# Kernel optimization log

Hardware: AMD Instinct MI355X
Metric: run time of the kernel (lower is better)

## Reference

```python
import jax, jax.numpy as jnp
import numpy as np

R = 16            # DFL bins (reg_max)
C = 80            # num classes
STRIDES = (8, 16, 32)
CONF = 0.25
IOU_T = 0.45
MAX_DET = 300
K_PRE = 1024      # fixed pre-NMS candidate count (static-shape stand-in for torch's boolean mask)
CLS_OFFSET = 4096.0  # > max image coord; class-aware NMS offset (torchvision batched_nms trick)


def setup_inputs() -> dict:
    key = jax.random.key(0)
    k0, k1, k2 = jax.random.split(key, 3)
    B, CH = 16, 4 * R + C
    return {
        "p0": jax.random.normal(k0, (B, CH, 80, 80), jnp.float32),
        "p1": jax.random.normal(k1, (B, CH, 40, 40), jnp.float32),
        "p2": jax.random.normal(k2, (B, CH, 20, 20), jnp.float32),
        "h_img": 640,
        "w_img": 640,
    }


def _decode_level(p, stride):
    # p: (B, 4R+C, H, W)
    B, _, H, W = p.shape
    box_logits = p[:, : 4 * R].reshape(B, 4, R, H * W)
    bins = jnp.arange(R, dtype=p.dtype)
    # DFLIntegral: softmax over bins, expectation -> l,t,r,b distances (in stride units)
    ltrb = jnp.einsum('bkrm,r->bkm', jax.nn.softmax(box_logits, axis=2), bins) * stride  # (B,4,HW)
    yv, xv = jnp.meshgrid(jnp.arange(H, dtype=p.dtype), jnp.arange(W, dtype=p.dtype), indexing='ij')
    cx = (xv.reshape(-1) + 0.5) * stride  # (HW,)
    cy = (yv.reshape(-1) + 0.5) * stride
    x1 = cx[None] - ltrb[:, 0]
    y1 = cy[None] - ltrb[:, 1]
    x2 = cx[None] + ltrb[:, 2]
    y2 = cy[None] + ltrb[:, 3]
    boxes = jnp.stack((x1, y1, x2, y2), axis=2)  # (B, HW, 4)
    scores = jax.nn.sigmoid(p[:, 4 * R:].reshape(B, C, H * W))  # (B, C, HW)
    smax = scores.max(axis=1)      # (B, HW)
    labels = scores.argmax(axis=1)  # (B, HW) int
    return boxes, smax, labels


def _pairwise_iou(b):
    # b: (K, 4) xyxy
    area = (b[:, 2] - b[:, 0]) * (b[:, 3] - b[:, 1])
    lt = jnp.maximum(b[:, None, :2], b[None, :, :2])
    rb = jnp.minimum(b[:, None, 2:], b[None, :, 2:])
    wh = jnp.clip(rb - lt, 0.0)
    inter = wh[..., 0] * wh[..., 1]
    return inter / (area[:, None] + area[None, :] - inter + 1e-7)


def _nms_single(boxes, smax, labels):
    # boxes (A,4), smax (A,), labels (A,)
    s = jnp.where(smax > CONF, smax, -1.0)
    sv, idx = jax.lax.top_k(s, K_PRE)          # score-sorted pre-NMS candidates
    bsel = boxes[idx]                           # (K,4)
    lsel = labels[idx]
    vsel = sv > CONF                            # candidate passes conf filter
    boff = bsel + lsel[:, None].astype(bsel.dtype) * CLS_OFFSET  # class-aware offset
    iou = _pairwise_iou(boff)
    iou = iou * (1.0 - jnp.eye(K_PRE, dtype=iou.dtype))  # no self-suppression

    def step(supp, i):
        keep_i = jnp.logical_and(~supp[i], vsel[i])
        supp = jnp.where(keep_i, supp | (iou[i] > IOU_T), supp)
        return supp, keep_i

    _, keep = jax.lax.scan(step, jnp.zeros(K_PRE, bool), jnp.arange(K_PRE))
    rank = jnp.cumsum(keep) - 1
    slot = jnp.where(keep & (rank < MAX_DET), rank, MAX_DET)  # dump overflow into dummy slot
    boxes_out = jnp.zeros((MAX_DET + 1, 4), bsel.dtype).at[slot].set(bsel)[:MAX_DET]
    scores_out = jnp.zeros((MAX_DET + 1,), sv.dtype).at[slot].set(sv)[:MAX_DET]
    labels_out = jnp.full((MAX_DET + 1,), -1, jnp.int32).at[slot].set(lsel.astype(jnp.int32))[:MAX_DET]
    n = jnp.minimum(keep.sum(), MAX_DET)
    valid_out = jnp.arange(MAX_DET) < n
    return boxes_out, scores_out, labels_out, valid_out


def reference(p0, p1, p2, h_img, w_img):
    parts = [_decode_level(p, s) for p, s in zip((p0, p1, p2), STRIDES)]
    boxes = jnp.concatenate([x[0] for x in parts], axis=1)   # (B, A, 4)
    smax = jnp.concatenate([x[1] for x in parts], axis=1)    # (B, A)
    labels = jnp.concatenate([x[2] for x in parts], axis=1)  # (B, A)
    hi = jnp.array([w_img - 1, h_img - 1, w_img - 1, h_img - 1], boxes.dtype)
    boxes = jnp.clip(boxes, 0.0, hi)
    return jax.vmap(_nms_single)(boxes, smax, labels)
```

## Files before the change

### kernel.cpp

```cpp
#include <hip/hip_runtime.h>
#include <stdint.h>

#define NR 16
#define NC 80
#define NA 8400
#define NB 16
#define KPRE 1024
#define MAXDET 300
#define CONF_T 0.25f
#define IOU_THR 0.45f

__device__ __forceinline__ float read_dim(const void* p) {
  int iv = *(const int*)p;
  return (iv > 0 && iv < (1 << 20)) ? (float)iv : *(const float*)p;
}

__device__ __forceinline__ const float* level_ptr(const float* p0, const float* p1,
                                                  const float* p2, int a, int& HW,
                                                  int& W, float& stride, int& m) {
  if (a < 6400)      { HW = 6400; W = 80; stride = 8.f;  m = a;        return p0; }
  else if (a < 8000) { HW = 1600; W = 40; stride = 16.f; m = a - 6400; return p1; }
  else               { HW = 400;  W = 20; stride = 32.f; m = a - 8000; return p2; }
}

__device__ __forceinline__ uint64_t readlane64(uint64_t v, int lane) {
  uint32_t lo = (uint32_t)__builtin_amdgcn_readlane((int)(uint32_t)v, lane);
  uint32_t hi = (uint32_t)__builtin_amdgcn_readlane((int)(uint32_t)(v >> 32), lane);
  return ((uint64_t)hi << 32) | lo;
}

__global__ __launch_bounds__(256) void k_decode(
    const float* __restrict__ p0, const float* __restrict__ p1,
    const float* __restrict__ p2, const void* __restrict__ hp,
    const void* __restrict__ wp, float4* __restrict__ boxes,
    uint32_t* __restrict__ keys, int* __restrict__ labels) {
  int gid = blockIdx.x * 256 + threadIdx.x;
  if (gid >= NB * NA) return;
  int b = gid / NA, a = gid - b * NA;
  int HW, W, m; float stride;
  const float* p = level_ptr(p0, p1, p2, a, HW, W, stride, m);
  const float* base = p + (size_t)b * (4 * NR + NC) * HW + m;

  float d[4];
#pragma unroll
  for (int k = 0; k < 4; ++k) {
    float v[NR]; float mx = -3.4e38f;
#pragma unroll
    for (int r = 0; r < NR; ++r) { v[r] = base[(size_t)(k * NR + r) * HW]; mx = fmaxf(mx, v[r]); }
    float se = 0.f, sn = 0.f;
#pragma unroll
    for (int r = 0; r < NR; ++r) { float e = expf(v[r] - mx); se += e; sn += e * (float)r; }
    d[k] = sn / se * stride;
  }
  int x = m % W, y = m / W;
  float cx = ((float)x + 0.5f) * stride, cy = ((float)y + 0.5f) * stride;
  float hx = read_dim(wp) - 1.f, hy = read_dim(hp) - 1.f;
  boxes[gid] = make_float4(fminf(fmaxf(cx - d[0], 0.f), hx),
                           fminf(fmaxf(cy - d[1], 0.f), hy),
                           fminf(fmaxf(cx + d[2], 0.f), hx),
                           fminf(fmaxf(cy + d[3], 0.f), hy));

  const float* cls = base + (size_t)(4 * NR) * HW;
  float ml = cls[0]; int mc = 0;
#pragma unroll 4
  for (int c = 1; c < NC; ++c) {
    float v = cls[(size_t)c * HW];
    if (v > ml) { ml = v; mc = c; }
  }
  labels[gid] = mc;
  float smax = 1.f / (1.f + expf(-ml));
  float s = smax > CONF_T ? smax : -1.0f;
  uint32_t bt = __float_as_uint(s);
  keys[gid] = (bt & 0x80000000u) ? ~bt : (bt | 0x80000000u);
}

__global__ __launch_bounds__(1024) void k_selcomp(const uint32_t* __restrict__ keys,
                                                  uint64_t* __restrict__ cmp,
                                                  int* __restrict__ ccount) {
  __shared__ uint32_t skeys[NA];
  __shared__ uint32_t whist[16][256];
  __shared__ uint32_t hsum[256];
  __shared__ uint32_t ssuf[256];
  __shared__ int s_b1, s_rem, s_t16, s_cnt;
  int img = blockIdx.x;
  int tid = threadIdx.x;
  int w = tid >> 6, lane = tid & 63;
  const uint32_t* kb = keys + (size_t)img * NA;
  for (int j = tid; j < NA; j += 1024) skeys[j] = kb[j];
  if (tid == 0) s_cnt = 0;

  for (int j = tid; j < 16 * 256; j += 1024) ((uint32_t*)whist)[j] = 0;
  __syncthreads();
  for (int j = tid; j < NA; j += 1024) atomicAdd(&whist[w][skeys[j] >> 24], 1u);
  __syncthreads();
  if (tid < 256) { uint32_t s = 0; for (int i = 0; i < 16; ++i) s += whist[i][tid]; hsum[tid] = s; }
  __syncthreads();
  if (tid < 256) { uint32_t s = 0; for (int j = tid; j < 256; ++j) s += hsum[j]; ssuf[tid] = s; }
  __syncthreads();
  if (tid < 256) {
    uint32_t ab = (tid == 255) ? 0u : ssuf[tid + 1];
    if (ssuf[tid] >= KPRE && ab < KPRE) { s_b1 = tid; s_rem = KPRE - (int)ab; }
  }
  __syncthreads();
  int b1 = s_b1, rem = s_rem;
  __syncthreads();

  for (int j = tid; j < 16 * 256; j += 1024) ((uint32_t*)whist)[j] = 0;
  __syncthreads();
  for (int j = tid; j < NA; j += 1024) {
    uint32_t k = skeys[j];
    if ((int)(k >> 24) == b1) atomicAdd(&whist[w][(k >> 16) & 0xFF], 1u);
  }
  __syncthreads();
  if (tid < 256) { uint32_t s = 0; for (int i = 0; i < 16; ++i) s += whist[i][tid]; hsum[tid] = s; }
  __syncthreads();
  if (tid < 256) { uint32_t s = 0; for (int j = tid; j < 256; ++j) s += hsum[j]; ssuf[tid] = s; }
  __syncthreads();
  if (tid < 256) {
    int ab = (tid == 255) ? 0 : (int)ssuf[tid + 1];
    if ((int)ssuf[tid] >= rem && ab < rem) s_t16 = (b1 << 8) | tid;
  }
  __syncthreads();
  uint32_t t16 = (uint32_t)s_t16;

  for (int j0 = 0; j0 < NA; j0 += 1024) {
    int j = j0 + tid;
    uint32_t k = (j < NA) ? skeys[j] : 0;
    bool pass = (j < NA) && ((k >> 16) >= t16);
    uint64_t mask = __ballot(pass);
    int pre = __popcll(mask & ((1ull << lane) - 1ull));
    int wc = __popcll(mask);
    int base = 0;
    if (lane == 0) base = wc ? atomicAdd(&s_cnt, wc) : 0;
    base = __shfl(base, 0);
    if (pass)
      cmp[(size_t)img * NA + base + pre] =
          ((uint64_t)k << 32) | (uint64_t)(0xFFFFFFFFu - (uint32_t)j);
  }
  __syncthreads();
  if (tid == 0) ccount[img] = s_cnt;
}

__global__ __launch_bounds__(256) void k_rank2(
    const uint64_t* __restrict__ cmp, const int* __restrict__ ccount,
    const float4* __restrict__ boxes, const int* __restrict__ labels,
    float4* __restrict__ selbox, float4* __restrict__ selboff,
    float* __restrict__ selscore, int* __restrict__ sellab) {
  __shared__ uint64_t sk[2048];
  int img = blockIdx.y;
  int M = ccount[img]; if (M > NA) M = NA;
  if (blockIdx.x * 256 >= M) return;
  int c = blockIdx.x * 256 + threadIdx.x;
  uint64_t kc = (c < M) ? cmp[(size_t)img * NA + c] : 0;
  int rank = 0;
  for (int j0 = 0; j0 < M; j0 += 2048) {
    int nchunk = min(2048, M - j0);
    __syncthreads();
    for (int j = threadIdx.x; j < nchunk; j += 256)
      sk[j] = cmp[(size_t)img * NA + j0 + j];
    __syncthreads();
    if (c < M) {
      int j = 0;
      for (; j + 4 <= nchunk; j += 4) {
        rank += (int)(sk[j] > kc) + (int)(sk[j + 1] > kc) +
                (int)(sk[j + 2] > kc) + (int)(sk[j + 3] > kc);
      }
      for (; j < nchunk; ++j) rank += (int)(sk[j] > kc);
    }
  }
  if (c < M && rank < KPRE) {
    int a = (int)(0xFFFFFFFFu - (uint32_t)kc);
    uint32_t uk = (uint32_t)(kc >> 32);
    uint32_t bits = (uk & 0x80000000u) ? (uk & 0x7FFFFFFFu) : ~uk;
    float s = __uint_as_float(bits);
    int lab = labels[img * NA + a];
    float4 bx = boxes[img * NA + a];
    float off = (float)lab * 4096.0f;
    int o = img * KPRE + rank;
    selbox[o] = bx;
    selboff[o] = make_float4(bx.x + off, bx.y + off, bx.z + off, bx.w + off);
    selscore[o] = s;
    sellab[o] = lab;
  }
}

__global__ __launch_bounds__(256) void k_iou(const float4* __restrict__ selboff,
                                             uint64_t* __restrict__ rowmask) {
  __shared__ float4 bb[KPRE];
  int img = blockIdx.y;
  for (int j = threadIdx.x; j < KPRE; j += 256) bb[j] = selboff[img * KPRE + j];
  __syncthreads();
  int i = blockIdx.x * 16 + (threadIdx.x & 15);
  int w = threadIdx.x >> 4;
  float4 bi = bb[i];
  float ai = (bi.z - bi.x) * (bi.w - bi.y);
  uint64_t bits = 0;
  for (int jj = 0; jj < 64; ++jj) {
    int j = w * 64 + jj;
    float4 bj = bb[j];
    float lx = fmaxf(bi.x, bj.x), ly = fmaxf(bi.y, bj.y);
    float rx = fminf(bi.z, bj.z), ry = fminf(bi.w, bj.w);
    float iw = fmaxf(rx - lx, 0.f), ih = fmaxf(ry - ly, 0.f);
    float inter = iw * ih;
    float aj = (bj.z - bj.x) * (bj.w - bj.y);
    float iou = inter / (ai + aj - inter + 1e-7f);
    bits |= (uint64_t)((iou > IOU_THR) && (j != i)) << jj;
  }
  rowmask[(size_t)img * 16384 + (size_t)w * 1024 + i] = bits;
}

__global__ __launch_bounds__(64) void k_scan(
    const uint64_t* __restrict__ rowmask, const float4* __restrict__ selbox,
    const float* __restrict__ selscore, const int* __restrict__ sellab,
    float* __restrict__ out) {
  __shared__ float lsc[KPRE];
  __shared__ uint64_t buf[2][16 * 65];
  __shared__ int keepidx[MAXDET];
  int img = blockIdx.x, lane = threadIdx.x;
  const uint64_t* g = rowmask + (size_t)img * 16384;

  for (int j = lane; j < KPRE; j += 64) lsc[j] = selscore[img * KPRE + j];

  {
    uint64_t r0[16];
#pragma unroll
    for (int t = 0; t < 16; ++t) r0[t] = g[t * 1024 + lane];
#pragma unroll
    for (int t = 0; t < 16; ++t) buf[0][t * 65 + lane] = r0[t];
  }
  asm volatile("" ::: "memory");

  uint64_t remv = 0;
  int n = 0;
  for (int c = 0; c < 16; ++c) {
    uint64_t rn[16];
    if (c + 1 < 16) {
#pragma unroll
      for (int t = 0; t < 16; ++t) rn[t] = g[t * 1024 + (c + 1) * 64 + lane];
    }
    const uint64_t* B = buf[c & 1];
    uint64_t m = B[c * 65 + lane];
    float sc = lsc[c * 64 + lane];
    uint64_t vmask = __ballot(sc > CONF_T);
    uint64_t cur = readlane64(remv, c);
    uint64_t kmask = 0;
#pragma unroll
    for (int ii = 0; ii < 64; ++ii) {
      if (((vmask >> ii) & 1ull) && !((cur >> ii) & 1ull)) {
        cur |= readlane64(m, ii);
        kmask |= (1ull << ii);
        if (lane == 0 && n < MAXDET) keepidx[n] = c * 64 + ii;
        n++;
      }
    }
    if (lane < 16) {
      uint64_t km = kmask;
      while (km) {
        int ii2 = __ffsll((unsigned long long)km) - 1;
        km &= km - 1;
        remv |= B[lane * 65 + ii2];
      }
    }
    if (!((vmask >> 63) & 1ull) || n >= MAXDET) break;
    if (c + 1 < 16) {
#pragma unroll
      for (int t = 0; t < 16; ++t) buf[(c + 1) & 1][t * 65 + lane] = rn[t];
    }
    asm volatile("" ::: "memory");
  }

  asm volatile("" ::: "memory");
  float* ob = out;
  float* os = out + NB * MAXDET * 4;
  float* ol = out + NB * MAXDET * 5;
  float* ov = out + NB * MAXDET * 6;
  int nk = n < MAXDET ? n : MAXDET;
  for (int s0 = 0; s0 < MAXDET; s0 += 64) {
    int slot = s0 + lane;
    if (slot >= MAXDET) break;
    bool v = slot < nk;
    float4 bx = make_float4(0.f, 0.f, 0.f, 0.f);
    float scv = 0.f, lbv = -1.f;
    if (v) {
      int i = keepidx[slot];
      bx = selbox[img * KPRE + i];
      scv = lsc[i];
      lbv = (float)sellab[img * KPRE + i];
    }
    ((float4*)ob)[img * MAXDET + slot] = bx;
    os[img * MAXDET + slot] = scv;
    ol[img * MAXDET + slot] = lbv;
    ov[img * MAXDET + slot] = v ? 1.0f : 0.0f;
  }
}

extern "C" void kernel_launch(void* const* d_in, const int* in_sizes, int n_in,
                              void* d_out, int out_size, void* d_ws, size_t ws_size,
                              hipStream_t stream) {
  const float* p0 = (const float*)d_in[0];
  const float* p1 = (const float*)d_in[1];
  const float* p2 = (const float*)d_in[2];
  const void* hp = d_in[3];
  const void* wp = d_in[4];

  char* ws = (char*)d_ws;
  float4*   boxes    = (float4*)(ws + 0);
  uint64_t* rowmask  = (uint64_t*)(ws + 0);
  uint32_t* keys     = (uint32_t*)(ws + 2150400);
  int*      labels   = (int*)(ws + 2688000);
  float4*   selbox   = (float4*)(ws + 3225600);
  float4*   selboff  = (float4*)(ws + 3487744);
  float*    selscore = (float*)(ws + 3749888);
  int*      sellab   = (int*)(ws + 3815424);
  int*      ccount   = (int*)(ws + 3880960);
  uint64_t* cmp      = (uint64_t*)(ws + 3881024);

  k_decode<<<(NB * NA + 255) / 256, 256, 0, stream>>>(p0, p1, p2, hp, wp,
                                                      boxes, keys, labels);
  k_selcomp<<<NB, 1024, 0, stream>>>(keys, cmp, ccount);
  dim3 rg((NA + 255) / 256, NB);
  k_rank2<<<rg, 256, 0, stream>>>(cmp, ccount, boxes, labels,
                                  selbox, selboff, selscore, sellab);
  dim3 ig(KPRE / 16, NB);
  k_iou<<<ig, 256, 0, stream>>>(selboff, rowmask);
  k_scan<<<NB, 64, 0, stream>>>(rowmask, selbox, selscore, sellab,
                                (float*)d_out);
}
```

Baseline: 220.1 us.

## Split decode across four lanes per anchor and fuse rank into select kernel

The decode kernel now uses four threads per anchor. Each thread handles one DFL side and a strided quarter of the class channels, and the argmax and distances are combined with lane shuffles. This raises parallelism and memory-level concurrency in the bandwidth-heavy decode. The rank kernel is folded into the selection kernel: candidate keys and indices are compacted into shared memory and ranked there, which removes a launch and the global cmp round trip. The cost is that ranking for each image now runs on a single 1024-thread block, and candidates are capped at CMAX.

```diff
diff --git a/kernel.cpp b/kernel.cpp
--- a/kernel.cpp
+++ b/kernel.cpp
@@ -9,6 +9,7 @@
 #define MAXDET 300
 #define CONF_T 0.25f
 #define IOU_THR 0.45f
+#define CMAX 8184
 
 __device__ __forceinline__ float read_dim(const void* p) {
   int iv = *(const int*)p;
@@ -35,65 +36,77 @@
     const void* __restrict__ wp, float4* __restrict__ boxes,
     uint32_t* __restrict__ keys, int* __restrict__ labels) {
   int gid = blockIdx.x * 256 + threadIdx.x;
-  if (gid >= NB * NA) return;
-  int b = gid / NA, a = gid - b * NA;
+  int aid = gid >> 2, k = gid & 3;
+  int b = aid / NA, a = aid - b * NA;
   int HW, W, m; float stride;
   const float* p = level_ptr(p0, p1, p2, a, HW, W, stride, m);
   const float* base = p + (size_t)b * (4 * NR + NC) * HW + m;
 
-  float d[4];
-#pragma unroll
-  for (int k = 0; k < 4; ++k) {
-    float v[NR]; float mx = -3.4e38f;
-#pragma unroll
-    for (int r = 0; r < NR; ++r) { v[r] = base[(size_t)(k * NR + r) * HW]; mx = fmaxf(mx, v[r]); }
-    float se = 0.f, sn = 0.f;
-#pragma unroll
-    for (int r = 0; r < NR; ++r) { float e = expf(v[r] - mx); se += e; sn += e * (float)r; }
-    d[k] = sn / se * stride;
-  }
-  int x = m % W, y = m / W;
-  float cx = ((float)x + 0.5f) * stride, cy = ((float)y + 0.5f) * stride;
-  float hx = read_dim(wp) - 1.f, hy = read_dim(hp) - 1.f;
-  boxes[gid] = make_float4(fminf(fmaxf(cx - d[0], 0.f), hx),
-                           fminf(fmaxf(cy - d[1], 0.f), hy),
-                           fminf(fmaxf(cx + d[2], 0.f), hx),
-                           fminf(fmaxf(cy + d[3], 0.f), hy));
-
-  const float* cls = base + (size_t)(4 * NR) * HW;
-  float ml = cls[0]; int mc = 0;
+  float v[NR]; float mx = -3.4e38f;
+#pragma unroll
+  for (int r = 0; r < NR; ++r) { v[r] = base[(size_t)(k * NR + r) * HW]; mx = fmaxf(mx, v[r]); }
+  float se = 0.f, sn = 0.f;
+#pragma unroll
+  for (int r = 0; r < NR; ++r) { float e = expf(v[r] - mx); se += e; sn += e * (float)r; }
+  float dk = sn / se * stride;
+
+  float ml = -3.4e38f; int mc = NC;
 #pragma unroll 4
-  for (int c = 1; c < NC; ++c) {
-    float v = cls[(size_t)c * HW];
-    if (v > ml) { ml = v; mc = c; }
-  }
-  labels[gid] = mc;
-  float smax = 1.f / (1.f + expf(-ml));
-  float s = smax > CONF_T ? smax : -1.0f;
-  uint32_t bt = __float_as_uint(s);
-  keys[gid] = (bt & 0x80000000u) ? ~bt : (bt | 0x80000000u);
-}
-
-__global__ __launch_bounds__(1024) void k_selcomp(const uint32_t* __restrict__ keys,
-                                                  uint64_t* __restrict__ cmp,
-                                                  int* __restrict__ ccount) {
-  __shared__ uint32_t skeys[NA];
-  __shared__ uint32_t whist[16][256];
-  __shared__ uint32_t hsum[256];
-  __shared__ uint32_t ssuf[256];
+  for (int c = 0; c < 20; ++c) {
+    int ch = 4 * c + k;
+    float vv = base[(size_t)(4 * NR + ch) * HW];
+    if (vv > ml) { ml = vv; mc = ch; }
+  }
+#pragma unroll
+  for (int off = 1; off < 4; off <<= 1) {
+    float ov = __shfl_xor(ml, off);
+    int oc = __shfl_xor(mc, off);
+    if (ov > ml || (ov == ml && oc < mc)) { ml = ov; mc = oc; }
+  }
+  int lane = threadIdx.x & 63;
+  int bl = lane & ~3;
+  float dl = __shfl(dk, bl), dt = __shfl(dk, bl + 1);
+  float dr = __shfl(dk, bl + 2), db = __shfl(dk, bl + 3);
+
+  if (k == 0) {
+    int x = m % W, y = m / W;
+    float cx = ((float)x + 0.5f) * stride, cy = ((float)y + 0.5f) * stride;
+    float hx = read_dim(wp) - 1.f, hy = read_dim(hp) - 1.f;
+    boxes[aid] = make_float4(fminf(fmaxf(cx - dl, 0.f), hx),
+                             fminf(fmaxf(cy - dt, 0.f), hy),
+                             fminf(fmaxf(cx + dr, 0.f), hx),
+                             fminf(fmaxf(cy + db, 0.f), hy));
+  } else if (k == 1) {
+    float smax = 1.f / (1.f + expf(-ml));
+    float s = smax > CONF_T ? smax : -1.0f;
+    uint32_t bt = __float_as_uint(s);
+    keys[aid] = (bt & 0x80000000u) ? ~bt : (bt | 0x80000000u);
+  } else if (k == 2) {
+    labels[aid] = mc;
+  }
+}
+
+__global__ __launch_bounds__(1024) void k_selcomp(
+    const uint32_t* __restrict__ keys, const float4* __restrict__ boxes,
+    const int* __restrict__ labels, float4* __restrict__ selbox,
+    float4* __restrict__ selboff, float* __restrict__ selscore,
+    int* __restrict__ sellab) {
+  __shared__ __align__(16) uint32_t skeys[NA];
+  __shared__ uint32_t whist[8][256];
+  __shared__ uint32_t hsum[256], ssuf[256];
+  __shared__ __align__(16) uint16_t cidx[8192];
   __shared__ int s_b1, s_rem, s_t16, s_cnt;
-  int img = blockIdx.x;
-  int tid = threadIdx.x;
-  int w = tid >> 6, lane = tid & 63;
+  int img = blockIdx.x, tid = threadIdx.x;
+  int w2 = tid >> 7, lane = tid & 63;
   const uint32_t* kb = keys + (size_t)img * NA;
   for (int j = tid; j < NA; j += 1024) skeys[j] = kb[j];
   if (tid == 0) s_cnt = 0;
 
-  for (int j = tid; j < 16 * 256; j += 1024) ((uint32_t*)whist)[j] = 0;
-  __syncthreads();
-  for (int j = tid; j < NA; j += 1024) atomicAdd(&whist[w][skeys[j] >> 24], 1u);
-  __syncthreads();
-  if (tid < 256) { uint32_t s = 0; for (int i = 0; i < 16; ++i) s += whist[i][tid]; hsum[tid] = s; }
+  for (int j = tid; j < 8 * 256; j += 1024) ((uint32_t*)whist)[j] = 0;
+  __syncthreads();
+  for (int j = tid; j < NA; j += 1024) atomicAdd(&whist[w2][skeys[j] >> 24], 1u);
+  __syncthreads();
+  if (tid < 256) { uint32_t s = 0; for (int i = 0; i < 8; ++i) s += whist[i][tid]; hsum[tid] = s; }
   __syncthreads();
   if (tid < 256) { uint32_t s = 0; for (int j = tid; j < 256; ++j) s += hsum[j]; ssuf[tid] = s; }
   __syncthreads();
@@ -105,14 +118,14 @@
   int b1 = s_b1, rem = s_rem;
   __syncthreads();
 
-  for (int j = tid; j < 16 * 256; j += 1024) ((uint32_t*)whist)[j] = 0;
+  for (int j = tid; j < 8 * 256; j += 1024) ((uint32_t*)whist)[j] = 0;
   __syncthreads();
   for (int j = tid; j < NA; j += 1024) {
     uint32_t k = skeys[j];
-    if ((int)(k >> 24) == b1) atomicAdd(&whist[w][(k >> 16) & 0xFF], 1u);
-  }
-  __syncthreads();
-  if (tid < 256) { uint32_t s = 0; for (int i = 0; i < 16; ++i) s += whist[i][tid]; hsum[tid] = s; }
+    if ((int)(k >> 24) == b1) atomicAdd(&whist[w2][(k >> 16) & 0xFF], 1u);
+  }
+  __syncthreads();
+  if (tid < 256) { uint32_t s = 0; for (int i = 0; i < 8; ++i) s += whist[i][tid]; hsum[tid] = s; }
   __syncthreads();
   if (tid < 256) { uint32_t s = 0; for (int j = tid; j < 256; ++j) s += hsum[j]; ssuf[tid] = s; }
   __syncthreads();
@@ -123,64 +136,59 @@
   __syncthreads();
   uint32_t t16 = (uint32_t)s_t16;
 
+  uint32_t* ckey = skeys;
   for (int j0 = 0; j0 < NA; j0 += 1024) {
     int j = j0 + tid;
     uint32_t k = (j < NA) ? skeys[j] : 0;
     bool pass = (j < NA) && ((k >> 16) >= t16);
+    __syncthreads();
     uint64_t mask = __ballot(pass);
     int pre = __popcll(mask & ((1ull << lane) - 1ull));
     int wc = __popcll(mask);
     int base = 0;
     if (lane == 0) base = wc ? atomicAdd(&s_cnt, wc) : 0;
     base = __shfl(base, 0);
-    if (pass)
-      cmp[(size_t)img * NA + base + pre] =
-          ((uint64_t)k << 32) | (uint64_t)(0xFFFFFFFFu - (uint32_t)j);
-  }
-  __syncthreads();
-  if (tid == 0) ccount[img] = s_cnt;
-}
-
-__global__ __launch_bounds__(256) void k_rank2(
-    const uint64_t* __restrict__ cmp, const int* __restrict__ ccount,
-    const float4* __restrict__ boxes, const int* __restrict__ labels,
-    float4* __restrict__ selbox, float4* __restrict__ selboff,
-    float* __restrict__ selscore, int* __restrict__ sellab) {
-  __shared__ uint64_t sk[2048];
-  int img = blockIdx.y;
-  int M = ccount[img]; if (M > NA) M = NA;
-  if (blockIdx.x * 256 >= M) return;
-  int c = blockIdx.x * 256 + threadIdx.x;
-  uint64_t kc = (c < M) ? cmp[(size_t)img * NA + c] : 0;
-  int rank = 0;
-  for (int j0 = 0; j0 < M; j0 += 2048) {
-    int nchunk = min(2048, M - j0);
-    __syncthreads();
-    for (int j = threadIdx.x; j < nchunk; j += 256)
-      sk[j] = cmp[(size_t)img * NA + j0 + j];
-    __syncthreads();
-    if (c < M) {
-      int j = 0;
-      for (; j + 4 <= nchunk; j += 4) {
-        rank += (int)(sk[j] > kc) + (int)(sk[j + 1] > kc) +
-                (int)(sk[j + 2] > kc) + (int)(sk[j + 3] > kc);
-      }
-      for (; j < nchunk; ++j) rank += (int)(sk[j] > kc);
-    }
-  }
-  if (c < M && rank < KPRE) {
-    int a = (int)(0xFFFFFFFFu - (uint32_t)kc);
-    uint32_t uk = (uint32_t)(kc >> 32);
-    uint32_t bits = (uk & 0x80000000u) ? (uk & 0x7FFFFFFFu) : ~uk;
-    float s = __uint_as_float(bits);
-    int lab = labels[img * NA + a];
-    float4 bx = boxes[img * NA + a];
-    float off = (float)lab * 4096.0f;
-    int o = img * KPRE + rank;
-    selbox[o] = bx;
-    selboff[o] = make_float4(bx.x + off, bx.y + off, bx.z + off, bx.w + off);
-    selscore[o] = s;
-    sellab[o] = lab;
+    int slot = base + pre;
+    if (pass && slot < CMAX) { ckey[slot] = k; cidx[slot] = (uint16_t)j; }
+  }
+  __syncthreads();
+  int M = s_cnt; if (M > CMAX) M = CMAX;
+  if (tid < 8) { ckey[M + tid] = 0u; cidx[M + tid] = 0xFFFF; }
+  __syncthreads();
+
+  const uint4* ck4 = (const uint4*)ckey;
+  const uint4* ci8 = (const uint4*)cidx;
+  int G = (M + 7) >> 3;
+  for (int c = tid; c < M; c += 1024) {
+    uint32_t kc = ckey[c]; uint32_t ic = cidx[c];
+    int rank = 0;
+    for (int g = 0; g < G; ++g) {
+      uint4 ka = ck4[2 * g], kb4 = ck4[2 * g + 1];
+      uint4 q = ci8[g];
+      uint32_t i0 = q.x & 0xFFFFu, i1 = q.x >> 16, i2 = q.y & 0xFFFFu, i3 = q.y >> 16;
+      uint32_t i4 = q.z & 0xFFFFu, i5 = q.z >> 16, i6 = q.w & 0xFFFFu, i7 = q.w >> 16;
+      rank += (int)((ka.x > kc) || (ka.x == kc && i0 < ic));
+      rank += (int)((ka.y > kc) || (ka.y == kc && i1 < ic));
+      rank += (int)((ka.z > kc) || (ka.z == kc && i2 < ic));
+      rank += (int)((ka.w > kc) || (ka.w == kc && i3 < ic));
+      rank += (int)((kb4.x > kc) || (kb4.x == kc && i4 < ic));
+      rank += (int)((kb4.y > kc) || (kb4.y == kc && i5 < ic));
+      rank += (int)((kb4.z > kc) || (kb4.z == kc && i6 < ic));
+      rank += (int)((kb4.w > kc) || (kb4.w == kc && i7 < ic));
+    }
+    if (rank < KPRE) {
+      int a = (int)ic;
+      uint32_t bits = (kc & 0x80000000u) ? (kc & 0x7FFFFFFFu) : ~kc;
+      float s = __uint_as_float(bits);
+      int lab = labels[img * NA + a];
+      float4 bx = boxes[img * NA + a];
+      float off = (float)lab * 4096.0f;
+      int o = img * KPRE + rank;
+      selbox[o] = bx;
+      selboff[o] = make_float4(bx.x + off, bx.y + off, bx.z + off, bx.w + off);
+      selscore[o] = s;
+      sellab[o] = lab;
+    }
   }
 }
 
@@ -312,15 +320,11 @@
   float4*   selboff  = (float4*)(ws + 3487744);
   float*    selscore = (float*)(ws + 3749888);
   int*      sellab   = (int*)(ws + 3815424);
-  int*      ccount   = (int*)(ws + 3880960);
-  uint64_t* cmp      = (uint64_t*)(ws + 3881024);
-
-  k_decode<<<(NB * NA + 255) / 256, 256, 0, stream>>>(p0, p1, p2, hp, wp,
-                                                      boxes, keys, labels);
-  k_selcomp<<<NB, 1024, 0, stream>>>(keys, cmp, ccount);
-  dim3 rg((NA + 255) / 256, NB);
-  k_rank2<<<rg, 256, 0, stream>>>(cmp, ccount, boxes, labels,
-                                  selbox, selboff, selscore, sellab);
+
+  k_decode<<<(NB * NA * 4) / 256, 256, 0, stream>>>(p0, p1, p2, hp, wp,
+                                                    boxes, keys, labels);
+  k_selcomp<<<NB, 1024, 0, stream>>>(keys, boxes, labels,
+                                     selbox, selboff, selscore, sellab);
   dim3 ig(KPRE / 16, NB);
   k_iou<<<ig, 256, 0, stream>>>(selboff, rowmask);
   k_scan<<<NB, 64, 0, stream>>>(rowmask, selbox, selscore, sellab,
```

Result: slower. 246.8 us (+12.1%).

## Split decode per anchor across four lanes with shuffle reductions

Applied to the files above, without the earlier changes.

The decode kernel now assigns four threads to each anchor: each thread computes the DFL softmax for one box side and scans a strided quarter of the class channels, and a cross-lane shuffle reduction then recovers the max logit and its argmax. Lanes 0-2 write the box, key and label respectively. This raises thread-level parallelism and the number of loads in flight for the memory-bound decode, at the cost of less coalesced access per thread, since four adjacent lanes read the same anchor column, and extra shuffle work. The argmax tie-break takes the lowest channel index, which matches the original first-max semantics.

```diff
diff --git a/kernel.cpp b/kernel.cpp
--- a/kernel.cpp
+++ b/kernel.cpp
@@ -35,43 +35,54 @@
     const void* __restrict__ wp, float4* __restrict__ boxes,
     uint32_t* __restrict__ keys, int* __restrict__ labels) {
   int gid = blockIdx.x * 256 + threadIdx.x;
-  if (gid >= NB * NA) return;
-  int b = gid / NA, a = gid - b * NA;
+  int aid = gid >> 2, k = gid & 3;
+  int b = aid / NA, a = aid - b * NA;
   int HW, W, m; float stride;
   const float* p = level_ptr(p0, p1, p2, a, HW, W, stride, m);
   const float* base = p + (size_t)b * (4 * NR + NC) * HW + m;
 
-  float d[4];
-#pragma unroll
-  for (int k = 0; k < 4; ++k) {
-    float v[NR]; float mx = -3.4e38f;
-#pragma unroll
-    for (int r = 0; r < NR; ++r) { v[r] = base[(size_t)(k * NR + r) * HW]; mx = fmaxf(mx, v[r]); }
-    float se = 0.f, sn = 0.f;
-#pragma unroll
-    for (int r = 0; r < NR; ++r) { float e = expf(v[r] - mx); se += e; sn += e * (float)r; }
-    d[k] = sn / se * stride;
-  }
-  int x = m % W, y = m / W;
-  float cx = ((float)x + 0.5f) * stride, cy = ((float)y + 0.5f) * stride;
-  float hx = read_dim(wp) - 1.f, hy = read_dim(hp) - 1.f;
-  boxes[gid] = make_float4(fminf(fmaxf(cx - d[0], 0.f), hx),
-                           fminf(fmaxf(cy - d[1], 0.f), hy),
-                           fminf(fmaxf(cx + d[2], 0.f), hx),
-                           fminf(fmaxf(cy + d[3], 0.f), hy));
-
-  const float* cls = base + (size_t)(4 * NR) * HW;
-  float ml = cls[0]; int mc = 0;
+  float v[NR]; float mx = -3.4e38f;
+#pragma unroll
+  for (int r = 0; r < NR; ++r) { v[r] = base[(size_t)(k * NR + r) * HW]; mx = fmaxf(mx, v[r]); }
+  float se = 0.f, sn = 0.f;
+#pragma unroll
+  for (int r = 0; r < NR; ++r) { float e = expf(v[r] - mx); se += e; sn += e * (float)r; }
+  float dk = sn / se * stride;
+
+  float ml = -3.4e38f; int mc = NC;
 #pragma unroll 4
-  for (int c = 1; c < NC; ++c) {
-    float v = cls[(size_t)c * HW];
-    if (v > ml) { ml = v; mc = c; }
-  }
-  labels[gid] = mc;
-  float smax = 1.f / (1.f + expf(-ml));
-  float s = smax > CONF_T ? smax : -1.0f;
-  uint32_t bt = __float_as_uint(s);
-  keys[gid] = (bt & 0x80000000u) ? ~bt : (bt | 0x80000000u);
+  for (int c = 0; c < 20; ++c) {
+    int ch = 4 * c + k;
+    float vv = base[(size_t)(4 * NR + ch) * HW];
+    if (vv > ml) { ml = vv; mc = ch; }
+  }
+#pragma unroll
+  for (int off = 1; off < 4; off <<= 1) {
+    float ov = __shfl_xor(ml, off);
+    int oc = __shfl_xor(mc, off);
+    if (ov > ml || (ov == ml && oc < mc)) { ml = ov; mc = oc; }
+  }
+  int lane = threadIdx.x & 63;
+  int bl = lane & ~3;
+  float dl = __shfl(dk, bl), dt = __shfl(dk, bl + 1);
+  float dr = __shfl(dk, bl + 2), db = __shfl(dk, bl + 3);
+
+  if (k == 0) {
+    int x = m % W, y = m / W;
+    float cx = ((float)x + 0.5f) * stride, cy = ((float)y + 0.5f) * stride;
+    float hx = read_dim(wp) - 1.f, hy = read_dim(hp) - 1.f;
+    boxes[aid] = make_float4(fminf(fmaxf(cx - dl, 0.f), hx),
+                             fminf(fmaxf(cy - dt, 0.f), hy),
+                             fminf(fmaxf(cx + dr, 0.f), hx),
+                             fminf(fmaxf(cy + db, 0.f), hy));
+  } else if (k == 1) {
+    float smax = 1.f / (1.f + expf(-ml));
+    float s = smax > CONF_T ? smax : -1.0f;
+    uint32_t bt = __float_as_uint(s);
+    keys[aid] = (bt & 0x80000000u) ? ~bt : (bt | 0x80000000u);
+  } else if (k == 2) {
+    labels[aid] = mc;
+  }
 }
 
 __global__ __launch_bounds__(1024) void k_selcomp(const uint32_t* __restrict__ keys,
@@ -79,11 +90,9 @@
                                                   int* __restrict__ ccount) {
   __shared__ uint32_t skeys[NA];
   __shared__ uint32_t whist[16][256];
-  __shared__ uint32_t hsum[256];
-  __shared__ uint32_t ssuf[256];
+  __shared__ uint32_t hsum[256], ssuf[256];
   __shared__ int s_b1, s_rem, s_t16, s_cnt;
-  int img = blockIdx.x;
-  int tid = threadIdx.x;
+  int img = blockIdx.x, tid = threadIdx.x;
   int w = tid >> 6, lane = tid & 63;
   const uint32_t* kb = keys + (size_t)img * NA;
   for (int j = tid; j < NA; j += 1024) skeys[j] = kb[j];
@@ -315,8 +324,8 @@
   int*      ccount   = (int*)(ws + 3880960);
   uint64_t* cmp      = (uint64_t*)(ws + 3881024);
 
-  k_decode<<<(NB * NA + 255) / 256, 256, 0, stream>>>(p0, p1, p2, hp, wp,
-                                                      boxes, keys, labels);
+  k_decode<<<(NB * NA * 4) / 256, 256, 0, stream>>>(p0, p1, p2, hp, wp,
+                                                    boxes, keys, labels);
   k_selcomp<<<NB, 1024, 0, stream>>>(keys, cmp, ccount);
   dim3 rg((NA + 255) / 256, NB);
   k_rank2<<<rg, 256, 0, stream>>>(cmp, ccount, boxes, labels,
```

After: 207.1 us. 1.06x faster.
